# Optimization experiments

Hardware: AMD Instinct MI355X
Metric: run time of the kernel (lower is better)

Reference implementation:

```python
import jax, jax.numpy as jnp
import numpy as np

N_NODES = 100000
N_EDGES = 1600000
IN_C, HID_C, OUT_C = 128, 128, 40


def setup_inputs() -> dict:
    key = jax.random.key(0)
    ks = jax.random.split(key, 8)
    sd_in = 1.0 / np.sqrt(IN_C)
    sd_hid = 1.0 / np.sqrt(HID_C)
    return {
        "x": jax.random.normal(ks[0], (N_NODES, IN_C), dtype=jnp.float32),
        "edge_index": jax.random.randint(ks[1], (2, N_EDGES), 0, N_NODES, dtype=jnp.int64),
        # layer 1: lin_l (aggregated neighbors, with bias), lin_r (root, no bias)
        "W1l": jax.random.uniform(ks[2], (IN_C, HID_C), jnp.float32, -sd_in, sd_in),
        "W1r": jax.random.uniform(ks[3], (IN_C, HID_C), jnp.float32, -sd_in, sd_in),
        "b1": jnp.zeros((HID_C,), jnp.float32),
        # layer 2
        "W2l": jax.random.uniform(ks[4], (HID_C, OUT_C), jnp.float32, -sd_hid, sd_hid),
        "W2r": jax.random.uniform(ks[5], (HID_C, OUT_C), jnp.float32, -sd_hid, sd_hid),
        "b2": jnp.zeros((OUT_C,), jnp.float32),
    }


def _sage_conv(x, src, dst, Wl, Wr, b, num_nodes):
    # mean aggregation of source-node messages at destination nodes
    msg = x[src]                                          # [E, d] gather
    agg = jax.ops.segment_sum(msg, dst, num_segments=num_nodes)  # [N, d]
    cnt = jax.ops.segment_sum(jnp.ones((src.shape[0],), x.dtype), dst,
                              num_segments=num_nodes)     # [N]
    agg = agg / jnp.maximum(cnt, 1.0)[:, None]
    # lin_l(agg) + lin_r(x)  (bias lives in lin_l, matching PyG SAGEConv)
    return agg @ Wl + x @ Wr + b


def reference(x, edge_index, W1l, W1r, b1, W2l, W2r, b2):
    n = x.shape[0]
    src, dst = edge_index[0], edge_index[1]  # messages flow src -> dst
    h = jax.nn.relu(_sage_conv(x, src, dst, W1l, W1r, b1, n))
    # dropout p=0.0 -> identity
    out = _sage_conv(h, src, dst, W2l, W2r, b2, n)
    return jax.nn.log_softmax(out, axis=-1)
```

## Files before the change

kernel.cpp:

```cpp
#include <hip/hip_runtime.h>
#include <stdint.h>


typedef unsigned int uint32;
typedef unsigned short u16;
typedef __bf16 bf16x8 __attribute__((ext_vector_type(8)));
typedef float  f32x4  __attribute__((ext_vector_type(4)));
typedef unsigned short u16x8 __attribute__((ext_vector_type(8)));

#define CAPB 64
#define MAXE 2592
#define MAXN 104

__device__ __forceinline__ float bf2f(u16 u) {
    union { uint32 i; float f; } v; v.i = ((uint32)u) << 16; return v.f;
}
__device__ __forceinline__ u16 f2bf(float f) {
    union { float f; uint32 i; } v; v.f = f;
    uint32 i = v.i;
    uint32 r = (i + 0x7FFFu + ((i >> 16) & 1u)) >> 16;
    return (u16)r;
}

__global__ __launch_bounds__(256) void k_part1(const int* __restrict__ src,
        const int* __restrict__ dst, uint32* __restrict__ part,
        int* __restrict__ gcur, int E, int sw, uint32 magic, int cap) {
    __shared__ uint32 buf[1024];
    __shared__ int cnt8[8][8];
    __shared__ int base8[8][8];
    __shared__ int bstart[8], bn[8], gbase[8];
    int tid = threadIdx.x, rep = tid & 7;
    int ntiles = (E + 1023) >> 10;
    for (int tile = blockIdx.x; tile < ntiles; tile += gridDim.x) {
        if (tid < 64) cnt8[tid >> 3][tid & 7] = 0;
        __syncthreads();
        int e0 = (tile << 10) + tid * 4;
        int bk[4]; uint32 pk[4]; int nv = 0;
        if (e0 + 3 < E) {
            int4 d4 = *(const int4*)(dst + e0);
            int4 s4 = *(const int4*)(src + e0);
            int dd[4] = {d4.x, d4.y, d4.z, d4.w};
            int ss[4] = {s4.x, s4.y, s4.z, s4.w};
            nv = 4;
#pragma unroll
            for (int k = 0; k < 4; ++k) {
                bk[k] = (int)(((unsigned long long)(uint32)dd[k] * magic) >> 32);
                pk[k] = ((uint32)ss[k] << 14) | (uint32)(dd[k] - bk[k] * sw);
            }
        } else {
            for (int e = e0; e < E && e < e0 + 4; ++e) {
                int d = dst[e];
                int b = (int)(((unsigned long long)(uint32)d * magic) >> 32);
                bk[nv] = b;
                pk[nv] = ((uint32)src[e] << 14) | (uint32)(d - b * sw);
                ++nv;
            }
        }
        for (int k = 0; k < nv; ++k) atomicAdd(&cnt8[bk[k]][rep], 1);
        __syncthreads();
        if (tid == 0) {
            int run = 0;
            for (int b = 0; b < 8; ++b) {
                bstart[b] = run; int t0 = run;
                for (int r = 0; r < 8; ++r) { base8[b][r] = run; run += cnt8[b][r]; }
                bn[b] = run - t0;
            }
        }
        __syncthreads();
        if (tid < 64) cnt8[tid >> 3][tid & 7] = base8[tid >> 3][tid & 7];
        __syncthreads();
        for (int k = 0; k < nv; ++k) {
            int pos = atomicAdd(&cnt8[bk[k]][rep], 1);
            buf[pos] = pk[k];
        }
        if (tid < 8 && bn[tid] > 0)
            gbase[tid] = atomicAdd(&gcur[tid], bn[tid]);
        __syncthreads();
#pragma unroll
        for (int b = 0; b < 8; ++b) {
            int n = bn[b];
            if (n == 0) continue;
            int gb = gbase[b], bs = bstart[b];
            int lim = (b + 1) * cap;
            for (int i = tid; i < n; i += 256) {
                int p = gb + i;
                if (p < lim) part[p] = buf[bs + i];
            }
        }
        __syncthreads();
    }
}

__global__ __launch_bounds__(256) void k_part2(const uint32* __restrict__ part1,
        const int* __restrict__ gcur1, uint32* __restrict__ part2,
        int* __restrict__ gcur2, int cap1, int cap2, int sw2, uint32 magic2) {
    __shared__ uint32 buf[128][CAPB];
    __shared__ int lcnt[128], gbase[128];
    int s = blockIdx.x & 7;
    int m = gcur1[s] - s * cap1;
    const uint32* p1 = part1 + (size_t)s * cap1;
    int sbase = s * 128;
    int ntiles = (m + 1023) >> 10;
    for (int tile = blockIdx.x >> 3; tile < ntiles; tile += (gridDim.x >> 3)) {
        for (int i = threadIdx.x; i < 128; i += 256) lcnt[i] = 0;
        __syncthreads();
        int t0 = (tile << 10) + threadIdx.x * 4;
        if (t0 + 3 < m) {
            uint4 v4 = *(const uint4*)(p1 + t0);
            uint32 vv[4] = {v4.x, v4.y, v4.z, v4.w};
#pragma unroll
            for (int k = 0; k < 4; ++k) {
                uint32 dl = vv[k] & 16383u;
                int sub = (int)(((unsigned long long)dl * magic2) >> 32);
                uint32 pk = ((vv[k] >> 14) << 7) | (dl - (uint32)(sub * sw2));
                int slot = atomicAdd(&lcnt[sub], 1);
                if (slot < CAPB) buf[sub][slot] = pk;
                else {
                    int p = atomicAdd(&gcur2[sbase + sub], 1);
                    if (p < (sbase + sub + 1) * cap2) part2[p] = pk;
                }
            }
        } else {
            for (int idx = t0; idx < m && idx < t0 + 4; ++idx) {
                uint32 v = p1[idx];
                uint32 dl = v & 16383u;
                int sub = (int)(((unsigned long long)dl * magic2) >> 32);
                uint32 pk = ((v >> 14) << 7) | (dl - (uint32)(sub * sw2));
                int slot = atomicAdd(&lcnt[sub], 1);
                if (slot < CAPB) buf[sub][slot] = pk;
                else {
                    int p = atomicAdd(&gcur2[sbase + sub], 1);
                    if (p < (sbase + sub + 1) * cap2) part2[p] = pk;
                }
            }
        }
        __syncthreads();
        if (threadIdx.x < 128) {
            int n = min(lcnt[threadIdx.x], CAPB);
            lcnt[threadIdx.x] = n;
            if (n > 0) gbase[threadIdx.x] = atomicAdd(&gcur2[sbase + threadIdx.x], n);
        }
        __syncthreads();
        int b = threadIdx.x >> 1, halfsel = threadIdx.x & 1;
        int n = lcnt[b];
        if (n > 0) {
            int gb = gbase[b];
            int lim = (sbase + b + 1) * cap2;
            for (int i = halfsel; i < n; i += 2) {
                int p = gb + i;
                if (p < lim) part2[p] = buf[b][i];
            }
        }
        __syncthreads();
    }
}

__global__ void k_prep(const float* __restrict__ W1l, const float* __restrict__ W1r,
                       const float* __restrict__ W2l, const float* __restrict__ W2r,
                       u16* __restrict__ Wt1, u16* __restrict__ Wt2,
                       int* __restrict__ gcur1, int cap1,
                       int* __restrict__ gcur2, int cap2) {
    if (blockIdx.x == 0 && threadIdx.x < 8) gcur1[threadIdx.x] = threadIdx.x * cap1;
    if (blockIdx.x < 4) {
        int idx = blockIdx.x * 256 + threadIdx.x;
        gcur2[idx] = idx * cap2;
    }
    if (blockIdx.x < 128) {
        int idx = blockIdx.x * 256 + threadIdx.x;
        int c = idx >> 7, k = idx & 127;
        float v = (c < 128) ? W1l[k * 128 + c] : W1r[k * 128 + (c - 128)];
        Wt1[idx] = f2bf(v);
    } else {
        int idx = (blockIdx.x - 128) * 256 + threadIdx.x;
        int c = idx >> 7, k = idx & 127;
        const float* W = (c < 48) ? W2l : W2r;
        int cc = (c < 48) ? c : c - 48;
        float v = (cc < 40) ? W[k * 40 + cc] : 0.f;
        Wt2[idx] = f2bf(v);
    }
}

__global__ __launch_bounds__(512) void k_gemm1(const float* __restrict__ x,
        const u16* __restrict__ Wt,
        u16* __restrict__ z1, u16* __restrict__ r1, int N) {
    __shared__ u16 xs[128][136];
    int tid = threadIdx.x;
    int rbase = blockIdx.x * 128;
#pragma unroll
    for (int i = 0; i < 8; ++i) {
        int fi = tid + i * 512;
        int row = fi >> 5, c4 = fi & 31;
        int grow = rbase + row;
        grow = grow < N ? grow : N - 1;
        float4 v = *(const float4*)(x + ((size_t)grow << 7) + c4 * 4);
        ushort4 w4;
        w4.x = f2bf(v.x); w4.y = f2bf(v.y); w4.z = f2bf(v.z); w4.w = f2bf(v.w);
        *(ushort4*)&xs[row][c4 * 4] = w4;
    }

    int lane = tid & 63;
    int w    = tid >> 6;
    int l15 = lane & 15, g = lane >> 4;
    int rloc = (w >> 2) * 64;
    int cbase = (w & 3) * 64;

    bf16x8 Bf[4][4];
#pragma unroll
    for (int c = 0; c < 4; ++c)
#pragma unroll
        for (int ks = 0; ks < 4; ++ks)
            Bf[c][ks] = *(const bf16x8*)(Wt + (((size_t)(cbase + c * 16 + l15)) << 7)
                                            + ks * 32 + g * 8);

    f32x4 acc[4][4];
    f32x4 z4 = {0.f, 0.f, 0.f, 0.f};
#pragma unroll
    for (int r = 0; r < 4; ++r)
#pragma unroll
        for (int c = 0; c < 4; ++c) acc[r][c] = z4;

    __syncthreads();

#pragma unroll
    for (int ks = 0; ks < 4; ++ks) {
        bf16x8 Af[4];
#pragma unroll
        for (int r = 0; r < 4; ++r)
            Af[r] = *(const bf16x8*)&xs[rloc + r * 16 + l15][ks * 32 + g * 8];
#pragma unroll
        for (int r = 0; r < 4; ++r)
#pragma unroll
            for (int c = 0; c < 4; ++c)
                acc[r][c] = __builtin_amdgcn_mfma_f32_16x16x32_bf16(
                                Af[r], Bf[c][ks], acc[r][c], 0, 0, 0);
    }

#pragma unroll
    for (int r = 0; r < 4; ++r) {
#pragma unroll
        for (int c = 0; c < 4; ++c) {
            int col = cbase + c * 16 + l15;
            u16* out = (col < 128) ? z1 : r1;
            int cc = col & 127;
#pragma unroll
            for (int j = 0; j < 4; ++j) {
                int row = rbase + rloc + r * 16 + g * 4 + j;
                if (row < N) out[((size_t)row << 7) + cc] = f2bf(acc[r][c][j]);
            }
        }
    }
}

__global__ __launch_bounds__(256) void k_gemm2(const u16* __restrict__ hb,
        const u16* __restrict__ Wt2,
        u16* __restrict__ z2p, u16* __restrict__ r2, int N) {
    __shared__ u16 hs[128][136];
    int tid = threadIdx.x;
    int rbase = blockIdx.x * 128;
#pragma unroll
    for (int i = 0; i < 8; ++i) {
        int ci = tid + i * 256;
        int row = ci >> 4, c8 = ci & 15;
        int grow = rbase + row;
        grow = grow < N ? grow : N - 1;
        u16x8 v = *(const u16x8*)(hb + ((size_t)grow << 7) + c8 * 8);
        *(u16x8*)&hs[row][c8 * 8] = v;
    }

    int lane = tid & 63;
    int w    = tid >> 6;
    int l15 = lane & 15, g = lane >> 4;
    int rloc = (w >> 1) * 64;
    int half = w & 1;

    bf16x8 Bf[3][4];
#pragma unroll
    for (int c = 0; c < 3; ++c)
#pragma unroll
        for (int ks = 0; ks < 4; ++ks)
            Bf[c][ks] = *(const bf16x8*)(Wt2 + (((size_t)(half * 48 + c * 16 + l15)) << 7)
                                             + ks * 32 + g * 8);

    f32x4 acc[4][3];
    f32x4 z4 = {0.f, 0.f, 0.f, 0.f};
#pragma unroll
    for (int r = 0; r < 4; ++r)
#pragma unroll
        for (int c = 0; c < 3; ++c) acc[r][c] = z4;

    __syncthreads();

#pragma unroll
    for (int ks = 0; ks < 4; ++ks) {
        bf16x8 Af[4];
#pragma unroll
        for (int r = 0; r < 4; ++r)
            Af[r] = *(const bf16x8*)&hs[rloc + r * 16 + l15][ks * 32 + g * 8];
#pragma unroll
        for (int r = 0; r < 4; ++r)
#pragma unroll
            for (int c = 0; c < 3; ++c)
                acc[r][c] = __builtin_amdgcn_mfma_f32_16x16x32_bf16(
                                Af[r], Bf[c][ks], acc[r][c], 0, 0, 0);
    }

    if (half == 0) {
#pragma unroll
        for (int r = 0; r < 4; ++r)
#pragma unroll
            for (int c = 0; c < 3; ++c) {
                int col = c * 16 + l15;
#pragma unroll
                for (int j = 0; j < 4; ++j) {
                    int row = rbase + rloc + r * 16 + g * 4 + j;
                    if (row < N) z2p[((size_t)row << 6) + col] = f2bf(acc[r][c][j]);
                }
            }
        int row = rbase + rloc + lane;
        if (row < N) {
            u16x8 z8 = {0, 0, 0, 0, 0, 0, 0, 0};
            *(u16x8*)(z2p + ((size_t)row << 6) + 48) = z8;
            *(u16x8*)(z2p + ((size_t)row << 6) + 56) = z8;
        }
    } else {
#pragma unroll
        for (int r = 0; r < 4; ++r)
#pragma unroll
            for (int c = 0; c < 3; ++c) {
                int col = c * 16 + l15;
                if (col < 40) {
#pragma unroll
                    for (int j = 0; j < 4; ++j) {
                        int row = rbase + rloc + r * 16 + g * 4 + j;
                        if (row < N) r2[(size_t)row * 40 + col] = f2bf(acc[r][c][j]);
                    }
                }
            }
    }
}

__global__ __launch_bounds__(512) void k_agg1_f(const u16* __restrict__ z1,
        const u16* __restrict__ r1, const float* __restrict__ b1,
        const uint32* __restrict__ part2, const int* __restrict__ gcur2,
        u16* __restrict__ h, int N, int sw1, int sw2, int cap2) {
    __shared__ uint32 ebuf[MAXE];
    __shared__ uint32 esrt[MAXE];
    __shared__ int cnt[MAXN], cur[MAXN], rs[MAXN + 32];
    int b = blockIdx.x, s = b >> 7, sub = b & 127;
    int nb = s * sw1 + sub * sw2;
    int slice_end = min((s + 1) * sw1, N);
    int nn = min(sw2, slice_end - nb);
    if (nn <= 0) return;
    int tid = threadIdx.x;
    int m2 = gcur2[b] - b * cap2;
    m2 = min(m2, min(cap2, MAXE));
    const uint32* p2 = part2 + (size_t)b * cap2;

    for (int i = tid; i < m2; i += 512) ebuf[i] = p2[i];
    for (int i = tid; i < nn; i += 512) cnt[i] = 0;
    __syncthreads();
    for (int i = tid; i < m2; i += 512) atomicAdd(&cnt[ebuf[i] & 127], 1);
    __syncthreads();
    if (tid < 64) {
        int c0 = (tid < nn) ? cnt[tid] : 0;
        int c1 = (64 + tid < nn) ? cnt[64 + tid] : 0;
        for (int off = 1; off < 64; off <<= 1) {
            int t0 = __shfl_up(c0, off, 64);
            int t1 = __shfl_up(c1, off, 64);
            if (tid >= off) { c0 += t0; c1 += t1; }
        }
        int tot0 = __shfl(c0, 63, 64);
        if (tid == 0) rs[0] = 0;
        rs[tid + 1] = c0;
        rs[64 + tid + 1] = tot0 + c1;
    }
    __syncthreads();
    for (int i = tid; i < nn; i += 512) cur[i] = rs[i];
    __syncthreads();
    for (int i = tid; i < m2; i += 512) {
        uint32 v = ebuf[i];
        int pos = atomicAdd(&cur[v & 127], 1);
        esrt[pos] = v >> 7;
    }
    __syncthreads();

    int lane = tid & 63, wv = tid >> 6;
    int g = lane >> 4, c = lane & 15;
    for (int node = wv; node < nn; node += 8) {
        int s0 = rs[node], s1 = rs[node + 1];
        float acc[8];
#pragma unroll
        for (int i = 0; i < 8; ++i) acc[i] = 0.f;
        int j = s0 + g;
        for (; j + 12 < s1; j += 16) {
            int sA = esrt[j], sB = esrt[j + 4];
            int sC = esrt[j + 8], sD = esrt[j + 12];
            u16x8 a = *(const u16x8*)(z1 + ((size_t)sA << 7) + c * 8);
            u16x8 bb = *(const u16x8*)(z1 + ((size_t)sB << 7) + c * 8);
            u16x8 d = *(const u16x8*)(z1 + ((size_t)sC << 7) + c * 8);
            u16x8 e = *(const u16x8*)(z1 + ((size_t)sD << 7) + c * 8);
#pragma unroll
            for (int i = 0; i < 8; ++i)
                acc[i] += (bf2f(a[i]) + bf2f(bb[i])) + (bf2f(d[i]) + bf2f(e[i]));
        }
        for (; j + 4 < s1; j += 8) {
            int sA = esrt[j], sB = esrt[j + 4];
            u16x8 a = *(const u16x8*)(z1 + ((size_t)sA << 7) + c * 8);
            u16x8 bb = *(const u16x8*)(z1 + ((size_t)sB << 7) + c * 8);
#pragma unroll
            for (int i = 0; i < 8; ++i) acc[i] += bf2f(a[i]) + bf2f(bb[i]);
        }
        if (j < s1) {
            int sA = esrt[j];
            u16x8 a = *(const u16x8*)(z1 + ((size_t)sA << 7) + c * 8);
#pragma unroll
            for (int i = 0; i < 8; ++i) acc[i] += bf2f(a[i]);
        }
#pragma unroll
        for (int i = 0; i < 8; ++i) {
            acc[i] += __shfl_xor(acc[i], 16, 64);
            acc[i] += __shfl_xor(acc[i], 32, 64);
        }
        if (g == 0) {
            float inv = 1.0f / fmaxf((float)(s1 - s0), 1.0f);
            size_t go = ((size_t)(nb + node) << 7) + c * 8;
            u16x8 rv = *(const u16x8*)(r1 + go);
            float4 b0 = *(const float4*)(b1 + c * 8);
            float4 b4 = *(const float4*)(b1 + c * 8 + 4);
            float bbv[8] = {b0.x, b0.y, b0.z, b0.w, b4.x, b4.y, b4.z, b4.w};
            u16x8 o;
#pragma unroll
            for (int i = 0; i < 8; ++i)
                o[i] = f2bf(fmaxf(acc[i] * inv + bf2f(rv[i]) + bbv[i], 0.f));
            *(u16x8*)(h + go) = o;
        }
    }
}

__global__ __launch_bounds__(512) void k_agg2_f(const u16* __restrict__ z2p,
        const u16* __restrict__ r2, const float* __restrict__ b2,
        const uint32* __restrict__ part2, const int* __restrict__ gcur2,
        float* __restrict__ out, int N, int sw1, int sw2, int cap2) {
    __shared__ uint32 ebuf[MAXE];
    __shared__ uint32 esrt[MAXE];
    __shared__ int cnt[MAXN], cur[MAXN], rs[MAXN + 32];
    int b = blockIdx.x, s = b >> 7, sub = b & 127;
    int nb = s * sw1 + sub * sw2;
    int slice_end = min((s + 1) * sw1, N);
    int nn = min(sw2, slice_end - nb);
    if (nn <= 0) return;
    int tid = threadIdx.x;
    int m2 = gcur2[b] - b * cap2;
    m2 = min(m2, min(cap2, MAXE));
    const uint32* p2 = part2 + (size_t)b * cap2;

    for (int i = tid; i < m2; i += 512) ebuf[i] = p2[i];
    for (int i = tid; i < nn; i += 512) cnt[i] = 0;
    __syncthreads();
    for (int i = tid; i < m2; i += 512) atomicAdd(&cnt[ebuf[i] & 127], 1);
    __syncthreads();
    if (tid < 64) {
        int c0 = (tid < nn) ? cnt[tid] : 0;
        int c1 = (64 + tid < nn) ? cnt[64 + tid] : 0;
        for (int off = 1; off < 64; off <<= 1) {
            int t0 = __shfl_up(c0, off, 64);
            int t1 = __shfl_up(c1, off, 64);
            if (tid >= off) { c0 += t0; c1 += t1; }
        }
        int tot0 = __shfl(c0, 63, 64);
        if (tid == 0) rs[0] = 0;
        rs[tid + 1] = c0;
        rs[64 + tid + 1] = tot0 + c1;
    }
    __syncthreads();
    for (int i = tid; i < nn; i += 512) cur[i] = rs[i];
    __syncthreads();
    for (int i = tid; i < m2; i += 512) {
        uint32 v = ebuf[i];
        int pos = atomicAdd(&cur[v & 127], 1);
        esrt[pos] = v >> 7;
    }
    __syncthreads();

    int lane = tid & 63, wv = tid >> 6;
    int le = lane >> 3, c = lane & 7;
    bool act = c < 5;
    for (int node = wv; node < nn; node += 8) {
        int s0 = rs[node], s1 = rs[node + 1];
        float acc[8];
#pragma unroll
        for (int i = 0; i < 8; ++i) acc[i] = 0.f;
        int j = s0 + le;
        for (; j + 8 < s1; j += 16) {
            int sA = esrt[j], sB = esrt[j + 8];
            u16x8 a = *(const u16x8*)(z2p + ((size_t)sA << 6) + c * 8);
            u16x8 bb = *(const u16x8*)(z2p + ((size_t)sB << 6) + c * 8);
#pragma unroll
            for (int i = 0; i < 8; ++i) acc[i] += bf2f(a[i]) + bf2f(bb[i]);
        }
        if (j < s1) {
            int sA = esrt[j];
            u16x8 a = *(const u16x8*)(z2p + ((size_t)sA << 6) + c * 8);
#pragma unroll
            for (int i = 0; i < 8; ++i) acc[i] += bf2f(a[i]);
        }
#pragma unroll
        for (int i = 0; i < 8; ++i) {
            acc[i] += __shfl_xor(acc[i], 8, 64);
            acc[i] += __shfl_xor(acc[i], 16, 64);
            acc[i] += __shfl_xor(acc[i], 32, 64);
        }
        if (le == 0) {
            float inv = 1.0f / fmaxf((float)(s1 - s0), 1.0f);
            float v[8];
            if (act) {
                u16x8 rv = *(const u16x8*)(r2 + (size_t)(nb + node) * 40 + c * 8);
                float4 b0 = *(const float4*)(b2 + c * 8);
                float4 b4 = *(const float4*)(b2 + c * 8 + 4);
                float bbv[8] = {b0.x, b0.y, b0.z, b0.w, b4.x, b4.y, b4.z, b4.w};
#pragma unroll
                for (int i = 0; i < 8; ++i) v[i] = acc[i] * inv + bf2f(rv[i]) + bbv[i];
            } else {
#pragma unroll
                for (int i = 0; i < 8; ++i) v[i] = -1e30f;
            }
            float m = v[0];
#pragma unroll
            for (int i = 1; i < 8; ++i) m = fmaxf(m, v[i]);
            m = fmaxf(m, __shfl_xor(m, 1, 64));
            m = fmaxf(m, __shfl_xor(m, 2, 64));
            m = fmaxf(m, __shfl_xor(m, 4, 64));
            float sum = 0.f;
            if (act) {
#pragma unroll
                for (int i = 0; i < 8; ++i) sum += __expf(v[i] - m);
            }
            sum += __shfl_xor(sum, 1, 64);
            sum += __shfl_xor(sum, 2, 64);
            sum += __shfl_xor(sum, 4, 64);
            float lse = __logf(sum);
            if (act) {
                float4 o0, o4;
                o0.x = v[0] - m - lse; o0.y = v[1] - m - lse;
                o0.z = v[2] - m - lse; o0.w = v[3] - m - lse;
                o4.x = v[4] - m - lse; o4.y = v[5] - m - lse;
                o4.z = v[6] - m - lse; o4.w = v[7] - m - lse;
                *(float4*)(out + (size_t)(nb + node) * 40 + c * 8) = o0;
                *(float4*)(out + (size_t)(nb + node) * 40 + c * 8 + 4) = o4;
            }
        }
    }
}

extern "C" void kernel_launch(void* const* d_in, const int* in_sizes, int n_in,
                              void* d_out, int out_size, void* d_ws, size_t ws_size,
                              hipStream_t stream) {
    const float* x   = (const float*)d_in[0];
    const int*   ei  = (const int*)d_in[1];
    const float* W1l = (const float*)d_in[2];
    const float* W1r = (const float*)d_in[3];
    const float* b1  = (const float*)d_in[4];
    const float* W2l = (const float*)d_in[5];
    const float* W2r = (const float*)d_in[6];
    const float* b2  = (const float*)d_in[7];
    float* out = (float*)d_out;

    int N = in_sizes[0] / 128;
    int E = in_sizes[1] / 2;
    const int* esrc = ei;
    const int* edst = ei + E;

    int sw1 = (N + 7) / 8;
    int sw2 = (sw1 + 127) / 128;
    uint32 magic1 = (uint32)((((unsigned long long)1 << 32) + sw1 - 1) / sw1);
    uint32 magic2 = (uint32)((((unsigned long long)1 << 32) + sw2 - 1) / sw2);
    int cap1 = (((E >> 3) + 8192) + 3) & ~3;
    int cap2 = (((E >> 10) + 1024) + 3) & ~3;

    char* p = (char*)d_ws;
    size_t off = 0;
    auto alloc = [&](size_t bytes) {
        void* q = p + off;
        off = (off + bytes + 255) & ~(size_t)255;
        return q;
    };
    int* gcur1 = (int*)alloc(64);
    int* gcur2 = (int*)alloc(1024 * 4);
    u16* Wt1 = (u16*)alloc(256 * 128 * 2);
    u16* Wt2 = (u16*)alloc(96 * 128 * 2);
    uint32* part1 = (uint32*)alloc((size_t)8 * cap1 * 4);
    uint32* part2 = (uint32*)alloc((size_t)1024 * cap2 * 4);
    u16* z1 = (u16*)alloc((size_t)N * 128 * 2);
    u16* r1 = (u16*)alloc((size_t)N * 128 * 2);
    u16* hb = r1;
    u16* z2p = z1;
    u16* r2  = z1 + (size_t)N * 64;

    k_prep<<<176, 256, 0, stream>>>(W1l, W1r, W2l, W2r, Wt1, Wt2,
                                    gcur1, cap1, gcur2, cap2);
    k_part1<<<1024, 256, 0, stream>>>(esrc, edst, part1, gcur1, E, sw1, magic1, cap1);
    k_part2<<<1024, 256, 0, stream>>>(part1, gcur1, part2, gcur2, cap1, cap2,
                                      sw2, magic2);

    k_gemm1<<<(N + 127) / 128, 512, 0, stream>>>(x, Wt1, z1, r1, N);
    k_agg1_f<<<1024, 512, 0, stream>>>(z1, r1, b1, part2, gcur2, hb,
                                       N, sw1, sw2, cap2);
    k_gemm2<<<(N + 127) / 128, 256, 0, stream>>>(hb, Wt2, z2p, r2, N);
    k_agg2_f<<<1024, 512, 0, stream>>>(z2p, r2, b2, part2, gcur2, out,
                                       N, sw1, sw2, cap2);
}
```

Baseline: 200.3 us.

## Reuse layer-1 per-bucket CSR sort in layer-2 aggregation; enlarge part2 tiles

The layer-1 aggregation kernel now writes its sorted source indices back into part2 and stores row starts in a new global rsg buffer. The layer-2 aggregation loads these directly and skips its own count, scan and scatter sort. This removes redundant LDS atomics and barriers from the second pass but adds global writes in the first pass. Separately, k_part2 processes 2048-element tiles on a 784-block grid, which changes how work is spread across blocks.

Result: no change. 199.0 us (-0.6%).

```diff
diff --git a/kernel.cpp b/kernel.cpp
--- a/kernel.cpp
+++ b/kernel.cpp
@@ -11,6 +11,7 @@
 #define CAPB 64
 #define MAXE 2592
 #define MAXN 104
+#define RSST 112
 
 __device__ __forceinline__ float bf2f(u16 u) {
     union { uint32 i; float f; } v; v.i = ((uint32)u) << 16; return v.f;
@@ -100,37 +101,40 @@
     int m = gcur1[s] - s * cap1;
     const uint32* p1 = part1 + (size_t)s * cap1;
     int sbase = s * 128;
-    int ntiles = (m + 1023) >> 10;
+    int ntiles = (m + 2047) >> 11;
     for (int tile = blockIdx.x >> 3; tile < ntiles; tile += (gridDim.x >> 3)) {
         for (int i = threadIdx.x; i < 128; i += 256) lcnt[i] = 0;
         __syncthreads();
-        int t0 = (tile << 10) + threadIdx.x * 4;
-        if (t0 + 3 < m) {
-            uint4 v4 = *(const uint4*)(p1 + t0);
-            uint32 vv[4] = {v4.x, v4.y, v4.z, v4.w};
-#pragma unroll
-            for (int k = 0; k < 4; ++k) {
-                uint32 dl = vv[k] & 16383u;
-                int sub = (int)(((unsigned long long)dl * magic2) >> 32);
-                uint32 pk = ((vv[k] >> 14) << 7) | (dl - (uint32)(sub * sw2));
-                int slot = atomicAdd(&lcnt[sub], 1);
-                if (slot < CAPB) buf[sub][slot] = pk;
-                else {
-                    int p = atomicAdd(&gcur2[sbase + sub], 1);
-                    if (p < (sbase + sub + 1) * cap2) part2[p] = pk;
+#pragma unroll
+        for (int half = 0; half < 2; ++half) {
+            int t0 = (tile << 11) + half * 1024 + threadIdx.x * 4;
+            if (t0 + 3 < m) {
+                uint4 v4 = *(const uint4*)(p1 + t0);
+                uint32 vv[4] = {v4.x, v4.y, v4.z, v4.w};
+#pragma unroll
+                for (int k = 0; k < 4; ++k) {
+                    uint32 dl = vv[k] & 16383u;
+                    int sub = (int)(((unsigned long long)dl * magic2) >> 32);
+                    uint32 pk = ((vv[k] >> 14) << 7) | (dl - (uint32)(sub * sw2));
+                    int slot = atomicAdd(&lcnt[sub], 1);
+                    if (slot < CAPB) buf[sub][slot] = pk;
+                    else {
+                        int p = atomicAdd(&gcur2[sbase + sub], 1);
+                        if (p < (sbase + sub + 1) * cap2) part2[p] = pk;
+                    }
                 }
-            }
-        } else {
-            for (int idx = t0; idx < m && idx < t0 + 4; ++idx) {
-                uint32 v = p1[idx];
-                uint32 dl = v & 16383u;
-                int sub = (int)(((unsigned long long)dl * magic2) >> 32);
-                uint32 pk = ((v >> 14) << 7) | (dl - (uint32)(sub * sw2));
-                int slot = atomicAdd(&lcnt[sub], 1);
-                if (slot < CAPB) buf[sub][slot] = pk;
-                else {
-                    int p = atomicAdd(&gcur2[sbase + sub], 1);
-                    if (p < (sbase + sub + 1) * cap2) part2[p] = pk;
+            } else {
+                for (int idx = t0; idx < m && idx < t0 + 4; ++idx) {
+                    uint32 v = p1[idx];
+                    uint32 dl = v & 16383u;
+                    int sub = (int)(((unsigned long long)dl * magic2) >> 32);
+                    uint32 pk = ((v >> 14) << 7) | (dl - (uint32)(sub * sw2));
+                    int slot = atomicAdd(&lcnt[sub], 1);
+                    if (slot < CAPB) buf[sub][slot] = pk;
+                    else {
+                        int p = atomicAdd(&gcur2[sbase + sub], 1);
+                        if (p < (sbase + sub + 1) * cap2) part2[p] = pk;
+                    }
                 }
             }
         }
@@ -341,8 +345,9 @@
 
 __global__ __launch_bounds__(512) void k_agg1_f(const u16* __restrict__ z1,
         const u16* __restrict__ r1, const float* __restrict__ b1,
-        const uint32* __restrict__ part2, const int* __restrict__ gcur2,
-        u16* __restrict__ h, int N, int sw1, int sw2, int cap2) {
+        uint32* __restrict__ part2, const int* __restrict__ gcur2,
+        u16* __restrict__ h, int* __restrict__ rsg,
+        int N, int sw1, int sw2, int cap2) {
     __shared__ uint32 ebuf[MAXE];
     __shared__ uint32 esrt[MAXE];
     __shared__ int cnt[MAXN], cur[MAXN], rs[MAXN + 32];
@@ -354,7 +359,7 @@
     int tid = threadIdx.x;
     int m2 = gcur2[b] - b * cap2;
     m2 = min(m2, min(cap2, MAXE));
-    const uint32* p2 = part2 + (size_t)b * cap2;
+    uint32* p2 = part2 + (size_t)b * cap2;
 
     for (int i = tid; i < m2; i += 512) ebuf[i] = p2[i];
     for (int i = tid; i < nn; i += 512) cnt[i] = 0;
@@ -383,6 +388,9 @@
         esrt[pos] = v >> 7;
     }
     __syncthreads();
+
+    for (int i = tid; i < m2; i += 512) p2[i] = esrt[i];
+    for (int i = tid; i <= nn; i += 512) rsg[b * RSST + i] = rs[i];
 
     int lane = tid & 63, wv = tid >> 6;
     int g = lane >> 4, c = lane & 15;
@@ -440,10 +448,10 @@
 __global__ __launch_bounds__(512) void k_agg2_f(const u16* __restrict__ z2p,
         const u16* __restrict__ r2, const float* __restrict__ b2,
         const uint32* __restrict__ part2, const int* __restrict__ gcur2,
-        float* __restrict__ out, int N, int sw1, int sw2, int cap2) {
-    __shared__ uint32 ebuf[MAXE];
+        const int* __restrict__ rsg, float* __restrict__ out,
+        int N, int sw1, int sw2, int cap2) {
     __shared__ uint32 esrt[MAXE];
-    __shared__ int cnt[MAXN], cur[MAXN], rs[MAXN + 32];
+    __shared__ int rs[MAXN + 1];
     int b = blockIdx.x, s = b >> 7, sub = b & 127;
     int nb = s * sw1 + sub * sw2;
     int slice_end = min((s + 1) * sw1, N);
@@ -454,32 +462,8 @@
     m2 = min(m2, min(cap2, MAXE));
     const uint32* p2 = part2 + (size_t)b * cap2;
 
-    for (int i = tid; i < m2; i += 512) ebuf[i] = p2[i];
-    for (int i = tid; i < nn; i += 512) cnt[i] = 0;
-    __syncthreads();
-    for (int i = tid; i < m2; i += 512) atomicAdd(&cnt[ebuf[i] & 127], 1);
-    __syncthreads();
-    if (tid < 64) {
-        int c0 = (tid < nn) ? cnt[tid] : 0;
-        int c1 = (64 + tid < nn) ? cnt[64 + tid] : 0;
-        for (int off = 1; off < 64; off <<= 1) {
-            int t0 = __shfl_up(c0, off, 64);
-            int t1 = __shfl_up(c1, off, 64);
-            if (tid >= off) { c0 += t0; c1 += t1; }
-        }
-        int tot0 = __shfl(c0, 63, 64);
-        if (tid == 0) rs[0] = 0;
-        rs[tid + 1] = c0;
-        rs[64 + tid + 1] = tot0 + c1;
-    }
-    __syncthreads();
-    for (int i = tid; i < nn; i += 512) cur[i] = rs[i];
-    __syncthreads();
-    for (int i = tid; i < m2; i += 512) {
-        uint32 v = ebuf[i];
-        int pos = atomicAdd(&cur[v & 127], 1);
-        esrt[pos] = v >> 7;
-    }
+    for (int i = tid; i < m2; i += 512) esrt[i] = p2[i];
+    for (int i = tid; i <= nn; i += 512) rs[i] = rsg[b * RSST + i];
     __syncthreads();
 
     int lane = tid & 63, wv = tid >> 6;
@@ -586,6 +570,7 @@
     };
     int* gcur1 = (int*)alloc(64);
     int* gcur2 = (int*)alloc(1024 * 4);
+    int* rsg   = (int*)alloc((size_t)1024 * RSST * 4);
     u16* Wt1 = (u16*)alloc(256 * 128 * 2);
     u16* Wt2 = (u16*)alloc(96 * 128 * 2);
     uint32* part1 = (uint32*)alloc((size_t)8 * cap1 * 4);
@@ -599,13 +584,13 @@
     k_prep<<<176, 256, 0, stream>>>(W1l, W1r, W2l, W2r, Wt1, Wt2,
                                     gcur1, cap1, gcur2, cap2);
     k_part1<<<1024, 256, 0, stream>>>(esrc, edst, part1, gcur1, E, sw1, magic1, cap1);
-    k_part2<<<1024, 256, 0, stream>>>(part1, gcur1, part2, gcur2, cap1, cap2,
-                                      sw2, magic2);
+    k_part2<<<784, 256, 0, stream>>>(part1, gcur1, part2, gcur2, cap1, cap2,
+                                     sw2, magic2);
 
     k_gemm1<<<(N + 127) / 128, 512, 0, stream>>>(x, Wt1, z1, r1, N);
-    k_agg1_f<<<1024, 512, 0, stream>>>(z1, r1, b1, part2, gcur2, hb,
+    k_agg1_f<<<1024, 512, 0, stream>>>(z1, r1, b1, part2, gcur2, hb, rsg,
                                        N, sw1, sw2, cap2);
     k_gemm2<<<(N + 127) / 128, 256, 0, stream>>>(hb, Wt2, z2p, r2, N);
-    k_agg2_f<<<1024, 512, 0, stream>>>(z2p, r2, b2, part2, gcur2, out,
+    k_agg2_f<<<1024, 512, 0, stream>>>(z2p, r2, b2, part2, gcur2, rsg, out,
                                        N, sw1, sw2, cap2);
 }
```
